# Kernel tuning notes

Measured on AMD Instinct MI355X. Metric: run time of the kernel, lower is better.

The kernel has to match this reference:

```python
import jax, jax.numpy as jnp
import numpy as np

B, T, H = 128, 1024, 512


def setup_inputs() -> dict:
    key = jax.random.key(0)
    ks = jax.random.split(key, 4)
    vel = jax.random.normal(ks[0], (B, T, 2), dtype=jnp.float32)
    # weight_ih ~ N(0, sqrt(1/2)); weight_hh orthogonal; biases zero; output zeroed
    # (we use random output weights so fwd output is non-trivial for testing)
    W_ih = jax.random.normal(ks[1], (H, 2), dtype=jnp.float32) * np.sqrt(0.5)
    A = jax.random.normal(ks[2], (H, H), dtype=jnp.float32)
    Q, _ = jnp.linalg.qr(A)
    W_hh = Q.astype(jnp.float32)
    b_ih = jnp.zeros((H,), dtype=jnp.float32)
    b_hh = jnp.zeros((H,), dtype=jnp.float32)
    W_out = jax.random.normal(ks[3], (2, H), dtype=jnp.float32) * 0.05
    b_out = jnp.zeros((2,), dtype=jnp.float32)
    return {"vel": vel, "W_ih": W_ih, "W_hh": W_hh, "b_ih": b_ih,
            "b_hh": b_hh, "W_out": W_out, "b_out": b_out}


def reference(vel, W_ih, W_hh, b_ih, b_hh, W_out, b_out):
    # Precompute input projection for all timesteps: [B, T, H]
    x_proj = jnp.einsum('btc,hc->bth', vel, W_ih) + b_ih + b_hh
    x_tbh = jnp.swapaxes(x_proj, 0, 1)  # [T, B, H] for scan over time

    def step(h, x_t):
        # h: [B, H]; x_t: [B, H]
        h_new = jnp.tanh(x_t + h @ W_hh.T)
        return h_new, h_new

    h0 = jnp.zeros((vel.shape[0], W_hh.shape[0]), dtype=vel.dtype)
    _, u_tbh = jax.lax.scan(step, h0, x_tbh)
    u_vals = jnp.swapaxes(u_tbh, 0, 1)  # [B, T, H]
    pos_est = jnp.einsum('bth,oh->bto', u_vals, W_out) + b_out  # [B, T, 2]
    return pos_est, u_vals
```

## Files before the change

### kernel.cpp

```cpp
#include <hip/hip_runtime.h>
#include <hip/hip_bf16.h>


#define TT 1024
#define BB 128
#define HH 512

typedef short s16x8 __attribute__((ext_vector_type(8)));
typedef float f32x4 __attribute__((ext_vector_type(4)));
typedef unsigned int uint;
typedef unsigned short ushort_t;

#define MFMA_B16(a, b, c) __builtin_amdgcn_mfma_f32_16x16x32_bf16((a), (b), (c), 0, 0, 0)

static __device__ __forceinline__ ushort_t bf16_rne(float f) {
  uint u = __float_as_uint(f);
  u += 0x7fffu + ((u >> 16) & 1u);
  return (ushort_t)(u >> 16);
}

static __device__ __forceinline__ uint cvt_pk_bf16(float lo, float hi) {
  uint r;
  asm("v_cvt_pk_bf16_f32 %0, %1, %2" : "=v"(r) : "v"(lo), "v"(hi));
  return r;
}

static __device__ __forceinline__ float tanh_fast(float z) {
  float e = __expf(2.0f * z);
  return 1.0f - 2.0f * __builtin_amdgcn_rcpf(e + 1.0f);
}

static __device__ __forceinline__ s16x8 packW(const float* wp) {
  float4 lo = *(const float4*)wp;
  float4 hi = *(const float4*)(wp + 4);
  s16x8 s;
  s[0] = (short)bf16_rne(lo.x); s[1] = (short)bf16_rne(lo.y);
  s[2] = (short)bf16_rne(lo.z); s[3] = (short)bf16_rne(lo.w);
  s[4] = (short)bf16_rne(hi.x); s[5] = (short)bf16_rne(hi.y);
  s[6] = (short)bf16_rne(hi.z); s[7] = (short)bf16_rne(hi.w);
  return s;
}

__global__ __launch_bounds__(512, 2) void rnn_kernel(
    const float* __restrict__ vel, const float* __restrict__ W_ih,
    const float* __restrict__ W_hh, const float* __restrict__ b_ih,
    const float* __restrict__ b_hh, float* __restrict__ u_out) {
  __shared__ uint4 lds_mem[9216];
  char* hlds = (char*)lds_mem;

  const int tid = threadIdx.x;
  const int lane = tid & 63;
  const int w = tid >> 6;
  const int c = blockIdx.x;
  const int l15 = lane & 15;
  const int kg = lane >> 4;
  const int n0w = w * 64;

  s16x8 wreg[4][12];
#pragma unroll
  for (int nt = 0; nt < 4; ++nt) {
    const float* wb = W_hh + (size_t)(n0w + nt * 16 + l15) * HH + kg * 8;
#pragma unroll
    for (int kt = 0; kt < 12; ++kt) wreg[nt][kt] = packW(wb + kt * 32);
  }

#pragma unroll
  for (int kti = 0; kti < 4; ++kti)
#pragma unroll
    for (int kq = 0; kq < 4; ++kq) {
      s16x8 s = packW(W_hh + (size_t)tid * HH + (12 + kti) * 32 + kq * 8);
      *(s16x8*)(hlds + 16384 + (kq * 4 + kti) * 8192 + tid * 16) = s;
    }

  float wihA[4], wihB[4], bsv[4];
#pragma unroll
  for (int nt = 0; nt < 4; ++nt) {
    int n = n0w + nt * 16 + l15;
    wihA[nt] = W_ih[n * 2 + 0];
    wihB[nt] = W_ih[n * 2 + 1];
    bsv[nt] = b_ih[n] + b_hh[n];
  }

  {
    uint4 z = {0u, 0u, 0u, 0u};
    *(uint4*)(hlds + tid * 32) = z;
    *(uint4*)(hlds + tid * 32 + 16) = z;
  }
  __syncthreads();

  const uint aswz = ((uint)l15 & 7u) << 4;
  const uint abase = (uint)l15 * 1024u + (uint)kg * 16u;
  const char* pAe = hlds + (abase ^ aswz);
  const char* pAo = hlds + ((abase + 64u) ^ aswz);
  const char* pW = hlds + 16384 + kg * 32768 + (n0w + l15) * 16;

  const bool odd = (l15 & 1) != 0;
  const uint rowb0 = (uint)(kg * 4) + (odd ? 2u : 0u);
  const uint rowb1 = rowb0 + 1u;
  const uint wr0 = rowb0 * 1024u + (uint)(n0w + (l15 & ~1)) * 2u;
  const uint wr1 = rowb1 * 1024u + (uint)(n0w + (l15 & ~1)) * 2u;
  const uint swz0 = (rowb0 & 7u) << 4;
  const uint swz1 = (rowb1 & 7u) << 4;

  uint uoff[4], voff[4];
#pragma unroll
  for (int r = 0; r < 4; ++r) {
    uint row = (uint)(c * 16 + kg * 4 + r);
    uoff[r] = row * (uint)(TT * HH) + (uint)(n0w + l15);
    voff[r] = row * (uint)(TT * 2);
  }

#define LDA(kt) ((kt & 1) ? *(const s16x8*)(pAo + ((kt) >> 1) * 128) \
                          : *(const s16x8*)(pAe + ((kt) >> 1) * 128))

  const f32x4 z4 = {0.f, 0.f, 0.f, 0.f};

  for (int t = 0; t < TT; ++t) {
    const float* vb = vel + t * 2;
    float2 v0 = *(const float2*)(vb + voff[0]);
    float2 v1 = *(const float2*)(vb + voff[1]);
    float2 v2 = *(const float2*)(vb + voff[2]);
    float2 v3 = *(const float2*)(vb + voff[3]);

    f32x4 acc0 = z4, acc1 = z4, acc2 = z4, acc3 = z4;

    s16x8 aF = LDA(0);
#pragma unroll
    for (int kt = 0; kt < 16; ++kt) {
      s16x8 aN;
      if (kt < 15) aN = LDA(kt + 1);
      s16x8 b0, b1, b2, b3;
      if (kt < 12) {
        b0 = wreg[0][kt]; b1 = wreg[1][kt]; b2 = wreg[2][kt]; b3 = wreg[3][kt];
      } else {
        const char* wp = pW + (kt - 12) * 8192;
        b0 = *(const s16x8*)(wp);
        b1 = *(const s16x8*)(wp + 256);
        b2 = *(const s16x8*)(wp + 512);
        b3 = *(const s16x8*)(wp + 768);
      }
      acc0 = MFMA_B16(aF, b0, acc0);
      acc1 = MFMA_B16(aF, b1, acc1);
      acc2 = MFMA_B16(aF, b2, acc2);
      acc3 = MFMA_B16(aF, b3, acc3);
      aF = aN;
    }

    float* ub = u_out + (size_t)t * HH;
    uint pr0v[4], pr1v[4];
#pragma unroll
    for (int nt = 0; nt < 4; ++nt) {
      f32x4 acc = (nt == 0) ? acc0 : (nt == 1) ? acc1 : (nt == 2) ? acc2 : acc3;
      float uvr[4];
      float2 vv[4] = {v0, v1, v2, v3};
#pragma unroll
      for (int r = 0; r < 4; ++r) {
        float x = fmaf(vv[r].x, wihA[nt], fmaf(vv[r].y, wihB[nt], bsv[nt]));
        uvr[r] = tanh_fast(x + acc[r]);
        __builtin_nontemporal_store(uvr[r], ub + uoff[r] + nt * 16);
      }
      uint a01 = cvt_pk_bf16(uvr[0], uvr[1]);
      uint a23 = cvt_pk_bf16(uvr[2], uvr[3]);
      uint b01 = __shfl_xor(a01, 1);
      uint b23 = __shfl_xor(a23, 1);
      uint eP = odd ? b23 : a01;
      uint oP = odd ? a23 : b01;
      pr0v[nt] = (eP & 0xFFFFu) | (oP << 16);
      pr1v[nt] = (eP >> 16) | (oP & 0xFFFF0000u);
    }

    asm volatile("s_barrier" ::: "memory");

#pragma unroll
    for (int nt = 0; nt < 4; ++nt) {
      *(uint*)(hlds + ((wr0 + (uint)(nt * 32)) ^ swz0)) = pr0v[nt];
      *(uint*)(hlds + ((wr1 + (uint)(nt * 32)) ^ swz1)) = pr1v[nt];
    }
    asm volatile("s_waitcnt lgkmcnt(0)" ::: "memory");
    __builtin_amdgcn_sched_barrier(0);
    asm volatile("s_barrier" ::: "memory");
  }
}

__global__ __launch_bounds__(256) void pos_kernel(const float* __restrict__ u,
                                                  const float* __restrict__ W_out,
                                                  const float* __restrict__ b_out,
                                                  float* __restrict__ pos) {
  int row = blockIdx.x * 4 + (threadIdx.x >> 6);
  int lane = threadIdx.x & 63;
  const float* ur = u + (size_t)row * HH + lane * 8;
  float4 u0 = *(const float4*)ur;
  float4 u1 = *(const float4*)(ur + 4);
  float4 w00 = *(const float4*)(W_out + lane * 8);
  float4 w01 = *(const float4*)(W_out + lane * 8 + 4);
  float4 w10 = *(const float4*)(W_out + HH + lane * 8);
  float4 w11 = *(const float4*)(W_out + HH + lane * 8 + 4);
  float p0 = u0.x * w00.x + u0.y * w00.y + u0.z * w00.z + u0.w * w00.w +
             u1.x * w01.x + u1.y * w01.y + u1.z * w01.z + u1.w * w01.w;
  float p1 = u0.x * w10.x + u0.y * w10.y + u0.z * w10.z + u0.w * w10.w +
             u1.x * w11.x + u1.y * w11.y + u1.z * w11.z + u1.w * w11.w;
#pragma unroll
  for (int off = 32; off; off >>= 1) {
    p0 += __shfl_xor(p0, off);
    p1 += __shfl_xor(p1, off);
  }
  if (lane == 0) {
    pos[(size_t)row * 2 + 0] = p0 + b_out[0];
    pos[(size_t)row * 2 + 1] = p1 + b_out[1];
  }
}

extern "C" void kernel_launch(void* const* d_in, const int* in_sizes, int n_in,
                              void* d_out, int out_size, void* d_ws, size_t ws_size,
                              hipStream_t stream) {
  const float* vel   = (const float*)d_in[0];
  const float* W_ih  = (const float*)d_in[1];
  const float* W_hh  = (const float*)d_in[2];
  const float* b_ih  = (const float*)d_in[3];
  const float* b_hh  = (const float*)d_in[4];
  const float* W_out = (const float*)d_in[5];
  const float* b_out = (const float*)d_in[6];

  float* pos = (float*)d_out;
  float* u   = pos + (size_t)BB * TT * 2;

  rnn_kernel<<<8, 512, 0, stream>>>(vel, W_ih, W_hh, b_ih, b_hh, u);
  pos_kernel<<<(BB * TT) / 4, 256, 0, stream>>>(u, W_out, b_out, pos);
}
```

Before: 2.685 ms.

## Halve RNN block to 4 waves each computing 128 hidden columns

Each of the 8 blocks now uses 256 threads (4 waves) instead of 512, and each wave owns 128 output columns (8 MFMA N-tiles) instead of 64. This doubles the register-resident W_hh slice per wave and interleaves LDS-sourced k-tiles with register ones through a reordered k loop. The aim is to cut per-step barrier cost and wave count per serial timestep while raising MFMA work per wave. The trade-offs are much higher register pressure with a possible spill risk (96 s16x8 weight registers plus 8 accumulators) and less latency hiding from fewer waves.

```diff
diff --git a/kernel.cpp b/kernel.cpp
--- a/kernel.cpp
+++ b/kernel.cpp
@@ -41,7 +41,7 @@
   return s;
 }
 
-__global__ __launch_bounds__(512, 2) void rnn_kernel(
+__global__ __launch_bounds__(256, 1) void rnn_kernel(
     const float* __restrict__ vel, const float* __restrict__ W_ih,
     const float* __restrict__ W_hh, const float* __restrict__ b_ih,
     const float* __restrict__ b_hh, float* __restrict__ u_out) {
@@ -54,11 +54,11 @@
   const int c = blockIdx.x;
   const int l15 = lane & 15;
   const int kg = lane >> 4;
-  const int n0w = w * 64;
-
-  s16x8 wreg[4][12];
-#pragma unroll
-  for (int nt = 0; nt < 4; ++nt) {
+  const int n0w = w * 128;
+
+  s16x8 wreg[8][12];
+#pragma unroll
+  for (int nt = 0; nt < 8; ++nt) {
     const float* wb = W_hh + (size_t)(n0w + nt * 16 + l15) * HH + kg * 8;
 #pragma unroll
     for (int kt = 0; kt < 12; ++kt) wreg[nt][kt] = packW(wb + kt * 32);
@@ -67,14 +67,17 @@
 #pragma unroll
   for (int kti = 0; kti < 4; ++kti)
 #pragma unroll
-    for (int kq = 0; kq < 4; ++kq) {
-      s16x8 s = packW(W_hh + (size_t)tid * HH + (12 + kti) * 32 + kq * 8);
-      *(s16x8*)(hlds + 16384 + (kq * 4 + kti) * 8192 + tid * 16) = s;
-    }
-
-  float wihA[4], wihB[4], bsv[4];
-#pragma unroll
-  for (int nt = 0; nt < 4; ++nt) {
+    for (int kq = 0; kq < 4; ++kq)
+#pragma unroll
+      for (int half = 0; half < 2; ++half) {
+        int n = tid + half * 256;
+        s16x8 s = packW(W_hh + (size_t)n * HH + (12 + kti) * 32 + kq * 8);
+        *(s16x8*)(hlds + 16384 + (kq * 4 + kti) * 8192 + n * 16) = s;
+      }
+
+  float wihA[8], wihB[8], bsv[8];
+#pragma unroll
+  for (int nt = 0; nt < 8; ++nt) {
     int n = n0w + nt * 16 + l15;
     wihA[nt] = W_ih[n * 2 + 0];
     wihB[nt] = W_ih[n * 2 + 1];
@@ -83,8 +86,8 @@
 
   {
     uint4 z = {0u, 0u, 0u, 0u};
-    *(uint4*)(hlds + tid * 32) = z;
-    *(uint4*)(hlds + tid * 32 + 16) = z;
+    uint4* zp = (uint4*)(hlds + tid * 64);
+    zp[0] = z; zp[1] = z; zp[2] = z; zp[3] = z;
   }
   __syncthreads();
 
@@ -102,61 +105,72 @@
   const uint swz0 = (rowb0 & 7u) << 4;
   const uint swz1 = (rowb1 & 7u) << 4;
 
-  uint uoff[4], voff[4];
-#pragma unroll
-  for (int r = 0; r < 4; ++r) {
-    uint row = (uint)(c * 16 + kg * 4 + r);
-    uoff[r] = row * (uint)(TT * HH) + (uint)(n0w + l15);
-    voff[r] = row * (uint)(TT * 2);
-  }
+  uint uoff[4];
+#pragma unroll
+  for (int r = 0; r < 4; ++r)
+    uoff[r] = (uint)(c * 16 + kg * 4 + r) * (uint)(TT * HH) + (uint)(n0w + l15);
+  const float* velb = vel + (size_t)(c * 16 + kg * 4) * (TT * 2);
 
 #define LDA(kt) ((kt & 1) ? *(const s16x8*)(pAo + ((kt) >> 1) * 128) \
                           : *(const s16x8*)(pAe + ((kt) >> 1) * 128))
 
   const f32x4 z4 = {0.f, 0.f, 0.f, 0.f};
+  const int ord[16] = {0, 1, 2, 12, 3, 4, 5, 13, 6, 7, 8, 14, 9, 10, 11, 15};
 
   for (int t = 0; t < TT; ++t) {
-    const float* vb = vel + t * 2;
-    float2 v0 = *(const float2*)(vb + voff[0]);
-    float2 v1 = *(const float2*)(vb + voff[1]);
-    float2 v2 = *(const float2*)(vb + voff[2]);
-    float2 v3 = *(const float2*)(vb + voff[3]);
-
-    f32x4 acc0 = z4, acc1 = z4, acc2 = z4, acc3 = z4;
-
-    s16x8 aF = LDA(0);
-#pragma unroll
-    for (int kt = 0; kt < 16; ++kt) {
+    const float* vb = velb + t * 2;
+    float2 v0 = *(const float2*)(vb);
+    float2 v1 = *(const float2*)(vb + 2048);
+    float2 v2 = *(const float2*)(vb + 4096);
+    float2 v3 = *(const float2*)(vb + 6144);
+
+    f32x4 acc[8] = {z4, z4, z4, z4, z4, z4, z4, z4};
+
+    s16x8 aF = LDA(ord[0]);
+#pragma unroll
+    for (int i = 0; i < 16; ++i) {
+      const int kt = ord[i];
       s16x8 aN;
-      if (kt < 15) aN = LDA(kt + 1);
-      s16x8 b0, b1, b2, b3;
+      if (i < 15) { const int kn = ord[i + 1]; aN = LDA(kn); }
       if (kt < 12) {
-        b0 = wreg[0][kt]; b1 = wreg[1][kt]; b2 = wreg[2][kt]; b3 = wreg[3][kt];
+#pragma unroll
+        for (int nt = 0; nt < 8; ++nt) acc[nt] = MFMA_B16(aF, wreg[nt][kt], acc[nt]);
       } else {
         const char* wp = pW + (kt - 12) * 8192;
-        b0 = *(const s16x8*)(wp);
-        b1 = *(const s16x8*)(wp + 256);
-        b2 = *(const s16x8*)(wp + 512);
-        b3 = *(const s16x8*)(wp + 768);
+        {
+          s16x8 b0 = *(const s16x8*)(wp);
+          s16x8 b1 = *(const s16x8*)(wp + 256);
+          s16x8 b2 = *(const s16x8*)(wp + 512);
+          s16x8 b3 = *(const s16x8*)(wp + 768);
+          acc[0] = MFMA_B16(aF, b0, acc[0]);
+          acc[1] = MFMA_B16(aF, b1, acc[1]);
+          acc[2] = MFMA_B16(aF, b2, acc[2]);
+          acc[3] = MFMA_B16(aF, b3, acc[3]);
+        }
+        {
+          s16x8 b4 = *(const s16x8*)(wp + 1024);
+          s16x8 b5 = *(const s16x8*)(wp + 1280);
+          s16x8 b6 = *(const s16x8*)(wp + 1536);
+          s16x8 b7 = *(const s16x8*)(wp + 1792);
+          acc[4] = MFMA_B16(aF, b4, acc[4]);
+          acc[5] = MFMA_B16(aF, b5, acc[5]);
+          acc[6] = MFMA_B16(aF, b6, acc[6]);
+          acc[7] = MFMA_B16(aF, b7, acc[7]);
+        }
       }
-      acc0 = MFMA_B16(aF, b0, acc0);
-      acc1 = MFMA_B16(aF, b1, acc1);
-      acc2 = MFMA_B16(aF, b2, acc2);
-      acc3 = MFMA_B16(aF, b3, acc3);
       aF = aN;
     }
 
     float* ub = u_out + (size_t)t * HH;
-    uint pr0v[4], pr1v[4];
-#pragma unroll
-    for (int nt = 0; nt < 4; ++nt) {
-      f32x4 acc = (nt == 0) ? acc0 : (nt == 1) ? acc1 : (nt == 2) ? acc2 : acc3;
+    uint pr0v[8], pr1v[8];
+#pragma unroll
+    for (int nt = 0; nt < 8; ++nt) {
       float uvr[4];
       float2 vv[4] = {v0, v1, v2, v3};
 #pragma unroll
       for (int r = 0; r < 4; ++r) {
         float x = fmaf(vv[r].x, wihA[nt], fmaf(vv[r].y, wihB[nt], bsv[nt]));
-        uvr[r] = tanh_fast(x + acc[r]);
+        uvr[r] = tanh_fast(x + acc[nt][r]);
         __builtin_nontemporal_store(uvr[r], ub + uoff[r] + nt * 16);
       }
       uint a01 = cvt_pk_bf16(uvr[0], uvr[1]);
@@ -172,7 +186,7 @@
     asm volatile("s_barrier" ::: "memory");
 
 #pragma unroll
-    for (int nt = 0; nt < 4; ++nt) {
+    for (int nt = 0; nt < 8; ++nt) {
       *(uint*)(hlds + ((wr0 + (uint)(nt * 32)) ^ swz0)) = pr0v[nt];
       *(uint*)(hlds + ((wr1 + (uint)(nt * 32)) ^ swz1)) = pr1v[nt];
     }
@@ -224,6 +238,6 @@
   float* pos = (float*)d_out;
   float* u   = pos + (size_t)BB * TT * 2;
 
-  rnn_kernel<<<8, 512, 0, stream>>>(vel, W_ih, W_hh, b_ih, b_hh, u);
+  rnn_kernel<<<8, 256, 0, stream>>>(vel, W_ih, W_hh, b_ih, b_hh, u);
   pos_kernel<<<(BB * TT) / 4, 256, 0, stream>>>(u, W_out, b_out, pos);
 }
```

Result: slower. 4.525 ms (+68.5%).
